# Performance work log

Measured on AMD Instinct MI355X. Metric: run time of the kernel, lower is better.

Reference implementation:

```python
import jax, jax.numpy as jnp
import numpy as np

EPS = 1e-06


def setup_inputs() -> dict:
    key = jax.random.key(0)
    kq, kk, kv = jax.random.split(key, 3)
    shape = (4, 16, 4096, 64)  # [batch, heads, seq, head_dim]
    q = jax.random.normal(kq, shape, dtype=jnp.float32)
    k = jax.random.normal(kk, shape, dtype=jnp.float32)
    v = jax.random.normal(kv, shape, dtype=jnp.float32)
    return {"q": q, "k": k, "v": v}


def reference(q, k, v):
    # elu(x)+1 feature map (positive kernel)
    q_prime = jax.nn.elu(q) + 1.0  # [b,h,s,d]
    k_prime = jax.nn.elu(k) + 1.0  # [b,h,s,d]
    # KV aggregate: [b,h,d,d] -- avoids the [s,s] score matrix
    kv_agg = jnp.einsum('bhsd,bhse->bhde', k_prime, v)
    num = jnp.einsum('bhsd,bhde->bhse', q_prime, kv_agg)  # [b,h,s,d]
    k_sum = k_prime.sum(axis=-2)                           # [b,h,d]
    denom = jnp.einsum('bhsd,bhd->bhs', q_prime, k_sum)[..., None] + EPS
    return num / denom
```

## Files before the change

### kernel.cpp

```cpp
#include <hip/hip_runtime.h>


#define EPS_LA 1e-6f

constexpr int BH = 64;
constexpr int SEQ = 4096;
constexpr int DIM = 64;
constexpr int KVELEM = DIM * DIM + DIM;
constexpr int NPB = 32;
constexpr int SCH = SEQ / NPB;

typedef short bf16x8 __attribute__((ext_vector_type(8)));
typedef float f32x4 __attribute__((ext_vector_type(4)));

__device__ __forceinline__ float elu1(float x) {
    return x > 0.f ? x + 1.f : __expf(x);
}
__device__ __forceinline__ void elu4(float4& v) {
    v.x = elu1(v.x); v.y = elu1(v.y); v.z = elu1(v.z); v.w = elu1(v.w);
}

__device__ __forceinline__ unsigned int f2bf(float x) {
    unsigned int u = __float_as_uint(x);
    return (u + 0x7fffu + ((u >> 16) & 1u)) >> 16;
}
__device__ __forceinline__ unsigned int pack2bf(float lo, float hi) {
    return f2bf(lo) | (f2bf(hi) << 16);
}

__device__ __forceinline__ int swz(int d, int s2) {
    return d * 64 + (s2 ^ (((d >> 1) & 7) << 2));
}

template<bool ATOMIC>
__global__ __launch_bounds__(256) void kv_mfma_kernel(
    const float* __restrict__ K, const float* __restrict__ V,
    float* __restrict__ dst) {
    const int bh = blockIdx.y;
    const int blk = blockIdx.x;
    const int t = threadIdx.x;
    const int w = t >> 6, l = t & 63;

    __shared__ unsigned int KT[64 * 64];
    __shared__ unsigned int VT[64 * 64];
    __shared__ float csumS[16][64];

    const float* Kb = K + ((size_t)bh * SEQ + (size_t)blk * SCH) * DIM;
    const float* Vb = V + ((size_t)bh * SEQ + (size_t)blk * SCH) * DIM;

    const int rg = t >> 4;
    const int c0 = (t & 15) * 4;

    float cs0 = 0.f, cs1 = 0.f, cs2 = 0.f, cs3 = 0.f;
    #pragma unroll
    for (int i = 0; i < 4; ++i) {
        const int s0 = 2 * rg + 32 * i;
        float4 ka = *(const float4*)(Kb + (size_t)s0 * DIM + c0);
        float4 kb = *(const float4*)(Kb + (size_t)(s0 + 1) * DIM + c0);
        const float4 va = *(const float4*)(Vb + (size_t)s0 * DIM + c0);
        const float4 vb = *(const float4*)(Vb + (size_t)(s0 + 1) * DIM + c0);
        elu4(ka); elu4(kb);
        cs0 += ka.x + kb.x; cs1 += ka.y + kb.y;
        cs2 += ka.z + kb.z; cs3 += ka.w + kb.w;
        const int s2 = s0 >> 1;
        KT[swz(c0 + 0, s2)] = pack2bf(ka.x, kb.x);
        KT[swz(c0 + 1, s2)] = pack2bf(ka.y, kb.y);
        KT[swz(c0 + 2, s2)] = pack2bf(ka.z, kb.z);
        KT[swz(c0 + 3, s2)] = pack2bf(ka.w, kb.w);
        VT[swz(c0 + 0, s2)] = pack2bf(va.x, vb.x);
        VT[swz(c0 + 1, s2)] = pack2bf(va.y, vb.y);
        VT[swz(c0 + 2, s2)] = pack2bf(va.z, vb.z);
        VT[swz(c0 + 3, s2)] = pack2bf(va.w, vb.w);
    }
    *(float4*)&csumS[rg][c0] = make_float4(cs0, cs1, cs2, cs3);
    __syncthreads();

    float* wout = ATOMIC ? dst + (size_t)bh * KVELEM
                         : dst + ((size_t)blk * BH + bh) * KVELEM;

    if (t < 64) {
        float s = 0.f;
        #pragma unroll
        for (int g = 0; g < 16; ++g) s += csumS[g][t];
        if (ATOMIC) atomicAdd(&wout[DIM * DIM + t], s);
        else        wout[DIM * DIM + t] = s;
    }

    f32x4 acc[4];
    #pragma unroll
    for (int m = 0; m < 4; ++m)
        #pragma unroll
        for (int r = 0; r < 4; ++r) acc[m][r] = 0.f;

    const int lg = l >> 4;
    const int lr = l & 15;
    #pragma unroll
    for (int ks = 0; ks < 4; ++ks) {
        const int s2b = 16 * ks + 4 * lg;
        const bf16x8 bfrag = *reinterpret_cast<const bf16x8*>(&VT[swz(16 * w + lr, s2b)]);
        #pragma unroll
        for (int m = 0; m < 4; ++m) {
            const bf16x8 afrag = *reinterpret_cast<const bf16x8*>(&KT[swz(16 * m + lr, s2b)]);
            acc[m] = __builtin_amdgcn_mfma_f32_16x16x32_bf16(afrag, bfrag, acc[m], 0, 0, 0);
        }
    }

    #pragma unroll
    for (int m = 0; m < 4; ++m) {
        #pragma unroll
        for (int r = 0; r < 4; ++r) {
            const int d = 16 * m + 4 * lg + r;
            const int e = 16 * w + lr;
            if (ATOMIC) atomicAdd(&wout[(size_t)d * DIM + e], acc[m][r]);
            else        wout[(size_t)d * DIM + e] = acc[m][r];
        }
    }
}

__global__ __launch_bounds__(256) void reduce_partials_kernel(
    const float* __restrict__ partial, float* __restrict__ fin) {
    const int bh = blockIdx.y;
    const int j = blockIdx.x * 256 + threadIdx.x;
    if (j >= KVELEM) return;
    float s = 0.f;
    #pragma unroll
    for (int c = 0; c < NPB; ++c)
        s += partial[((size_t)c * BH + bh) * KVELEM + j];
    fin[(size_t)bh * KVELEM + j] = s;
}

__global__ __launch_bounds__(256) void out_kernel(
    const float* __restrict__ Q, const float* __restrict__ ws,
    float* __restrict__ out) {
    const int bh = blockIdx.y;
    const int rb = blockIdx.x;
    const int wave = threadIdx.x >> 6, lane = threadIdx.x & 63;
    const int t = threadIdx.x;
    const int tr = lane >> 3;
    const int tc = lane & 7;

    const float* w = ws + (size_t)bh * KVELEM;
    const float* Qw = Q + ((size_t)bh * SEQ + (size_t)rb * 128 + (size_t)wave * 32) * DIM;
    float* Ow = out + ((size_t)bh * SEQ + (size_t)rb * 128 + (size_t)wave * 32) * DIM;

    __shared__ float kvS[DIM][DIM];
    __shared__ float ksumS[DIM];
    __shared__ float qS[4][32][DIM];

    #pragma unroll
    for (int i = 0; i < 4; ++i) {
        const int idx = (i * 256 + t) * 4;
        *(float4*)&kvS[idx >> 6][idx & 63] = *(const float4*)(w + idx);
    }
    if (t < DIM) ksumS[t] = w[DIM * DIM + t];

    #pragma unroll
    for (int it = 0; it < 8; ++it) {
        const int row = it * 4 + (lane >> 4);
        const int cc = lane & 15;
        float4 qv = *(const float4*)(Qw + (size_t)row * DIM + cc * 4);
        elu4(qv);
        *(float4*)&qS[wave][row][((cc ^ ((row >> 2) & 7)) & 15) * 4] = qv;
    }
    __syncthreads();

    float acc[4][8] = {{0.f}};
    float accd[4] = {0.f, 0.f, 0.f, 0.f};

    #pragma unroll 2
    for (int dc = 0; dc < 16; ++dc) {
        float4 qv[4];
        #pragma unroll
        for (int i = 0; i < 4; ++i)
            qv[i] = *(const float4*)&qS[wave][tr * 4 + i][((dc ^ tr) & 15) * 4];
        const float4 ks = *(const float4*)&ksumS[dc * 4];
        #pragma unroll
        for (int dd = 0; dd < 4; ++dd) {
            const int d = dc * 4 + dd;
            const float4 ka = *(const float4*)&kvS[d][tc * 8];
            const float4 kb = *(const float4*)&kvS[d][tc * 8 + 4];
            const float ksd = (&ks.x)[dd];
            #pragma unroll
            for (int i = 0; i < 4; ++i) {
                const float qq = (&qv[i].x)[dd];
                accd[i] += qq * ksd;
                acc[i][0] += qq * ka.x; acc[i][1] += qq * ka.y;
                acc[i][2] += qq * ka.z; acc[i][3] += qq * ka.w;
                acc[i][4] += qq * kb.x; acc[i][5] += qq * kb.y;
                acc[i][6] += qq * kb.z; acc[i][7] += qq * kb.w;
            }
        }
    }

    #pragma unroll
    for (int i = 0; i < 4; ++i) {
        const float inv = 1.f / (accd[i] + EPS_LA);
        float4 o0, o1;
        o0.x = acc[i][0] * inv; o0.y = acc[i][1] * inv;
        o0.z = acc[i][2] * inv; o0.w = acc[i][3] * inv;
        o1.x = acc[i][4] * inv; o1.y = acc[i][5] * inv;
        o1.z = acc[i][6] * inv; o1.w = acc[i][7] * inv;
        float* orow = Ow + (size_t)(tr * 4 + i) * DIM + tc * 8;
        *(float4*)(orow) = o0;
        *(float4*)(orow + 4) = o1;
    }
}

extern "C" void kernel_launch(void* const* d_in, const int* in_sizes, int n_in,
                              void* d_out, int out_size, void* d_ws, size_t ws_size,
                              hipStream_t stream) {
    const float* q = (const float*)d_in[0];
    const float* k = (const float*)d_in[1];
    const float* v = (const float*)d_in[2];
    float* out = (float*)d_out;
    float* ws = (float*)d_ws;

    const size_t partial_elems = (size_t)NPB * BH * KVELEM;
    const size_t need = (partial_elems + (size_t)BH * KVELEM) * sizeof(float);

    dim3 blk(256);
    const float* fin_ptr;
    if (ws_size >= need) {
        float* partial = ws;
        float* fin = ws + partial_elems;
        hipLaunchKernelGGL((kv_mfma_kernel<false>), dim3(NPB, BH), blk, 0, stream,
                           k, v, partial);
        hipLaunchKernelGGL(reduce_partials_kernel, dim3((KVELEM + 255) / 256, BH),
                           blk, 0, stream, partial, fin);
        fin_ptr = fin;
    } else {
        float* fin = ws;
        hipMemsetAsync(fin, 0, (size_t)BH * KVELEM * sizeof(float), stream);
        hipLaunchKernelGGL((kv_mfma_kernel<true>), dim3(NPB, BH), blk, 0, stream,
                           k, v, fin);
        fin_ptr = fin;
    }
    hipLaunchKernelGGL(out_kernel, dim3(SEQ / 128, BH), blk, 0, stream,
                       q, fin_ptr, out);
}
```

Baseline: 81.16 us.

## Split KV tile into two sub-tiles to halve LDS and raise occupancy

The KV aggregation kernel now stages its 128-row chunk as two 64-row sub-tiles, halving the K/V LDS buffers and accumulating MFMA results across them. The column-sum reduction moves to wave shuffles plus a 4-row LDS buffer, and the launch bound requests 6 blocks per SM. The swizzle is changed for the narrower rows to avoid bank conflicts. The aim is higher occupancy for this memory-bound phase, at the cost of an extra barrier per sub-tile and less load parallelism per pass.

Result: no change. 82.05 us (+1.1%).

```diff
diff --git a/kernel.cpp b/kernel.cpp
--- a/kernel.cpp
+++ b/kernel.cpp
@@ -8,6 +8,7 @@
 constexpr int DIM = 64;
 constexpr int KVELEM = DIM * DIM + DIM;
 constexpr int NPB = 32;
+constexpr int SUBT = 2;
 constexpr int SCH = SEQ / NPB;
 
 typedef short bf16x8 __attribute__((ext_vector_type(8)));
@@ -29,11 +30,11 @@
 }
 
 __device__ __forceinline__ int swz(int d, int s2) {
-    return d * 64 + (s2 ^ (((d >> 1) & 7) << 2));
+    return d * 32 + (s2 ^ ((((d >> 1) ^ (d >> 2)) & 7) << 2));
 }
 
 template<bool ATOMIC>
-__global__ __launch_bounds__(256) void kv_mfma_kernel(
+__global__ __launch_bounds__(256, 6) void kv_mfma_kernel(
     const float* __restrict__ K, const float* __restrict__ V,
     float* __restrict__ dst) {
     const int bh = blockIdx.y;
@@ -41,68 +42,82 @@
     const int t = threadIdx.x;
     const int w = t >> 6, l = t & 63;
 
-    __shared__ unsigned int KT[64 * 64];
-    __shared__ unsigned int VT[64 * 64];
-    __shared__ float csumS[16][64];
+    __shared__ unsigned int KT[64 * 32];
+    __shared__ unsigned int VT[64 * 32];
+    __shared__ float csumS[4][64];
 
     const float* Kb = K + ((size_t)bh * SEQ + (size_t)blk * SCH) * DIM;
     const float* Vb = V + ((size_t)bh * SEQ + (size_t)blk * SCH) * DIM;
 
-    const int rg = t >> 4;
     const int c0 = (t & 15) * 4;
+    const int lg = l >> 4;
+    const int lr = l & 15;
+
+    f32x4 acc[4];
+    #pragma unroll
+    for (int m = 0; m < 4; ++m)
+        #pragma unroll
+        for (int r = 0; r < 4; ++r) acc[m][r] = 0.f;
 
     float cs0 = 0.f, cs1 = 0.f, cs2 = 0.f, cs3 = 0.f;
-    #pragma unroll
-    for (int i = 0; i < 4; ++i) {
-        const int s0 = 2 * rg + 32 * i;
-        float4 ka = *(const float4*)(Kb + (size_t)s0 * DIM + c0);
-        float4 kb = *(const float4*)(Kb + (size_t)(s0 + 1) * DIM + c0);
-        const float4 va = *(const float4*)(Vb + (size_t)s0 * DIM + c0);
-        const float4 vb = *(const float4*)(Vb + (size_t)(s0 + 1) * DIM + c0);
-        elu4(ka); elu4(kb);
-        cs0 += ka.x + kb.x; cs1 += ka.y + kb.y;
-        cs2 += ka.z + kb.z; cs3 += ka.w + kb.w;
-        const int s2 = s0 >> 1;
-        KT[swz(c0 + 0, s2)] = pack2bf(ka.x, kb.x);
-        KT[swz(c0 + 1, s2)] = pack2bf(ka.y, kb.y);
-        KT[swz(c0 + 2, s2)] = pack2bf(ka.z, kb.z);
-        KT[swz(c0 + 3, s2)] = pack2bf(ka.w, kb.w);
-        VT[swz(c0 + 0, s2)] = pack2bf(va.x, vb.x);
-        VT[swz(c0 + 1, s2)] = pack2bf(va.y, vb.y);
-        VT[swz(c0 + 2, s2)] = pack2bf(va.z, vb.z);
-        VT[swz(c0 + 3, s2)] = pack2bf(va.w, vb.w);
-    }
-    *(float4*)&csumS[rg][c0] = make_float4(cs0, cs1, cs2, cs3);
-    __syncthreads();
+
+    #pragma unroll
+    for (int st = 0; st < SUBT; ++st) {
+        const float* Ks = Kb + (size_t)st * 64 * DIM;
+        const float* Vs = Vb + (size_t)st * 64 * DIM;
+
+        #pragma unroll
+        for (int i = 0; i < 2; ++i) {
+            const int p = (t >> 4) + 16 * i;
+            float4 ka = *(const float4*)(Ks + (size_t)(2 * p) * DIM + c0);
+            float4 kb = *(const float4*)(Ks + (size_t)(2 * p + 1) * DIM + c0);
+            const float4 va = *(const float4*)(Vs + (size_t)(2 * p) * DIM + c0);
+            const float4 vb = *(const float4*)(Vs + (size_t)(2 * p + 1) * DIM + c0);
+            elu4(ka); elu4(kb);
+            cs0 += ka.x + kb.x; cs1 += ka.y + kb.y;
+            cs2 += ka.z + kb.z; cs3 += ka.w + kb.w;
+            KT[swz(c0 + 0, p)] = pack2bf(ka.x, kb.x);
+            KT[swz(c0 + 1, p)] = pack2bf(ka.y, kb.y);
+            KT[swz(c0 + 2, p)] = pack2bf(ka.z, kb.z);
+            KT[swz(c0 + 3, p)] = pack2bf(ka.w, kb.w);
+            VT[swz(c0 + 0, p)] = pack2bf(va.x, vb.x);
+            VT[swz(c0 + 1, p)] = pack2bf(va.y, vb.y);
+            VT[swz(c0 + 2, p)] = pack2bf(va.z, vb.z);
+            VT[swz(c0 + 3, p)] = pack2bf(va.w, vb.w);
+        }
+
+        if (st == SUBT - 1) {
+            cs0 += __shfl_xor(cs0, 16); cs0 += __shfl_xor(cs0, 32);
+            cs1 += __shfl_xor(cs1, 16); cs1 += __shfl_xor(cs1, 32);
+            cs2 += __shfl_xor(cs2, 16); cs2 += __shfl_xor(cs2, 32);
+            cs3 += __shfl_xor(cs3, 16); cs3 += __shfl_xor(cs3, 32);
+            if (l < 16) *(float4*)&csumS[w][l * 4] = make_float4(cs0, cs1, cs2, cs3);
+        }
+        __syncthreads();
+
+        #pragma unroll
+        for (int ks = 0; ks < 2; ++ks) {
+            const int s2b = ks * 16 + lg * 4;
+            const bf16x8 bfrag =
+                *reinterpret_cast<const bf16x8*>(&VT[swz(16 * w + lr, s2b)]);
+            #pragma unroll
+            for (int m = 0; m < 4; ++m) {
+                const bf16x8 afrag =
+                    *reinterpret_cast<const bf16x8*>(&KT[swz(16 * m + lr, s2b)]);
+                acc[m] = __builtin_amdgcn_mfma_f32_16x16x32_bf16(afrag, bfrag, acc[m],
+                                                                 0, 0, 0);
+            }
+        }
+        if (st < SUBT - 1) __syncthreads();
+    }
 
     float* wout = ATOMIC ? dst + (size_t)bh * KVELEM
                          : dst + ((size_t)blk * BH + bh) * KVELEM;
 
     if (t < 64) {
-        float s = 0.f;
-        #pragma unroll
-        for (int g = 0; g < 16; ++g) s += csumS[g][t];
+        const float s = csumS[0][t] + csumS[1][t] + csumS[2][t] + csumS[3][t];
         if (ATOMIC) atomicAdd(&wout[DIM * DIM + t], s);
         else        wout[DIM * DIM + t] = s;
-    }
-
-    f32x4 acc[4];
-    #pragma unroll
-    for (int m = 0; m < 4; ++m)
-        #pragma unroll
-        for (int r = 0; r < 4; ++r) acc[m][r] = 0.f;
-
-    const int lg = l >> 4;
-    const int lr = l & 15;
-    #pragma unroll
-    for (int ks = 0; ks < 4; ++ks) {
-        const int s2b = 16 * ks + 4 * lg;
-        const bf16x8 bfrag = *reinterpret_cast<const bf16x8*>(&VT[swz(16 * w + lr, s2b)]);
-        #pragma unroll
-        for (int m = 0; m < 4; ++m) {
-            const bf16x8 afrag = *reinterpret_cast<const bf16x8*>(&KT[swz(16 * m + lr, s2b)]);
-            acc[m] = __builtin_amdgcn_mfma_f32_16x16x32_bf16(afrag, bfrag, acc[m], 0, 0, 0);
-        }
     }
 
     #pragma unroll
```
